# Optimization experiments

Measured on AMD Instinct MI355X. Metric: run time of the kernel, lower is better.

## Reference

```python
import jax, jax.numpy as jnp
import numpy as np

# Model config (matches init_kwargs)
DATA_L = 256
LATENT_L = 64
LATENT_N = 8
N_COMPS = 8
LOG_2PI = float(np.log(2.0 * np.pi))


def setup_inputs() -> dict:
    key = jax.random.key(0)
    ks = jax.random.split(key, 7)
    B = 2048
    N = B * LATENT_N  # 16384
    x = jax.random.normal(ks[0], (B, DATA_L), dtype=jnp.float32)
    W_e = jax.random.normal(ks[1], (DATA_L, LATENT_L * N_COMPS * 3), dtype=jnp.float32) * 0.05
    b_e = jnp.zeros((LATENT_L * N_COMPS * 3,), dtype=jnp.float32)
    W_d = jax.random.normal(ks[2], (LATENT_L, DATA_L * N_COMPS * 3), dtype=jnp.float32) * 0.05
    b_d = jnp.zeros((DATA_L * N_COMPS * 3,), dtype=jnp.float32)
    u_e = jax.random.normal(ks[3], (N, LATENT_L), dtype=jnp.float32)
    r = jax.random.uniform(ks[4], (N, LATENT_L), dtype=jnp.float32)
    return {"x": x, "W_e": W_e, "b_e": b_e, "W_d": W_d, "b_d": b_d, "u_e": u_e, "r": r}


def _split3(pred, K, D):
    # pred: (N, 3*K*D) -> m, logp, loga each (N, K, D)
    m = pred[:, : K * D].reshape(-1, K, D)
    logp = pred[:, K * D : 2 * K * D].reshape(-1, K, D)
    loga = pred[:, 2 * K * D :].reshape(-1, K, D)
    loga = jax.nn.log_softmax(loga, axis=1)  # loga - logsumexp over comps
    return m, logp, loga


def _discrete_sample(loga, r):
    # loga: (N, K, D), r: (N, D). Matches torch: idx = sum((r > cumsum(p)).int(), dim=1)
    c = jnp.cumsum(jnp.exp(loga), axis=1)  # (N, K, D)
    idx = jnp.sum((r[:, None, :] > c).astype(jnp.int32), axis=1)  # (N, D)
    return jnp.clip(idx, 0, loga.shape[1] - 1)


def reference(x, W_e, b_e, W_d, b_d, u_e, r):
    K, L, D = N_COMPS, LATENT_L, DATA_L
    x_rep = jnp.tile(x, (LATENT_N, 1))  # (N, D)

    # Encoder (KAN with width=[data_l, 3*K*L] modeled as dense layer)
    pred_e = x_rep @ W_e + b_e  # (N, 3*K*L)
    m_e, logp_e, loga_e = _split3(pred_e, K, L)

    # Sample mixture component per (row, latent dim), gather, reparameterize
    idx = _discrete_sample(loga_e, r)  # (N, L) int32
    m_sel = jnp.take_along_axis(m_e, idx[:, None, :], axis=1)[:, 0, :]  # (N, L)
    logp_sel = jnp.take_along_axis(logp_e, idx[:, None, :], axis=1)[:, 0, :]
    h = m_sel + jnp.exp(-0.5 * logp_sel) * u_e  # (N, L)

    # log q(h|x): mixture-of-Gaussians density at h
    uh = jnp.exp(0.5 * logp_e) * (h[:, None, :] - m_e)  # (N, K, L)
    L_e = jax.nn.logsumexp(loga_e - 0.5 * uh * uh + 0.5 * logp_e, axis=1)  # (N, L)
    L_e = -0.5 * L * LOG_2PI + jnp.sum(L_e, axis=1)  # (N,)

    # log prior N(0, I)
    L_q = -0.5 * L * LOG_2PI - 0.5 * jnp.sum(h * h, axis=1)  # (N,)

    # Decoder mixture likelihood of x
    pred_d = h @ W_d + b_d  # (N, 3*K*D)
    m_d, logp_d, loga_d = _split3(pred_d, K, D)
    ux = jnp.exp(0.5 * logp_d) * (x_rep[:, None, :] - m_d)  # (N, K, D)
    L_d = jax.nn.logsumexp(loga_d - 0.5 * ux * ux + 0.5 * logp_d, axis=1)  # (N, D)
    L_d = -0.5 * D * LOG_2PI + jnp.sum(L_d, axis=1)  # (N,)

    return -jnp.mean(L_d + L_q - L_e)
```

## Files before the change

kernel.cpp:

```cpp
#include <hip/hip_runtime.h>
#include <hip/hip_bf16.h>
#include <math.h>

#define D_L   256
#define L_L   64
#define K_C   8
#define BATCH 2048
#define NTOT  16384
#define ENC_COLS 1536
#define LOG2PI 1.8378770664093453f
#define L2E    1.4426950408889634f
#define LN2    0.6931471805599453f
#define C_HL2E 0.7213475204444817f

typedef __attribute__((ext_vector_type(8)))  short short8;
typedef __attribute__((ext_vector_type(8)))  unsigned short ushort8;
typedef __attribute__((ext_vector_type(4)))  unsigned short ushort4_;
typedef __attribute__((ext_vector_type(4)))  float float4_;
typedef __attribute__((ext_vector_type(16))) float float16_;

#if defined(__has_builtin)
#  if __has_builtin(__builtin_amdgcn_exp2f)
#    define EXP2F(x) __builtin_amdgcn_exp2f(x)
#  endif
#  if __has_builtin(__builtin_amdgcn_logf)
#    define LOG2F(x) __builtin_amdgcn_logf(x)
#  endif
#endif
#ifndef EXP2F
#  define EXP2F(x) __expf((x) * LN2)
#endif
#ifndef LOG2F
#  define LOG2F(x) (__logf(x) * L2E)
#endif

#define OFF_PE    0
#define OFF_H     (BATCH * ENC_COLS)
#define OFF_WET2  (OFF_H + NTOT * L_L / 2)
#define OFF_WDT2  (OFF_WET2 + ENC_COLS * D_L / 2)
#define OFF_ACC   (OFF_WDT2 + 6144 * 64 / 2)

#define DEC_BLOCKS (4 * (NTOT / 64))

__device__ __forceinline__ unsigned short f2bf(float f) {
  unsigned u = __float_as_uint(f);
  return (unsigned short)((u + 0x7fffu + ((u >> 16) & 1u)) >> 16);
}

__global__ __launch_bounds__(256) void k_prep(
    const float* __restrict__ We, const float* __restrict__ Wd,
    unsigned short* __restrict__ WeT2, unsigned short* __restrict__ WdT2,
    float* __restrict__ accf)
{
  const int bid = blockIdx.x, t = threadIdx.x;
  if (bid == 192) {
    if (t == 0) { accf[0] = 0.0f; *(unsigned*)(accf + 1) = 0u; }
    return;
  }

  const float* src; int C, rowbase, colbase; float scale;
  unsigned short* dst;
  if (bid < 96) {
    const int comp = bid / 12, p = (bid % 12) >> 2, dt = bid & 3;
    src = Wd; C = 6144; rowbase = 0;
    colbase = p * 2048 + comp * 256 + dt * 64;
    scale = p ? L2E : 1.0f;
    dst = WdT2 + (size_t)bid * 4096;
  } else {
    const int idx = bid - 96;
    src = We; C = ENC_COLS; rowbase = (idx & 3) * 64;
    colbase = (idx >> 2) * 64;
    scale = 1.0f;
    dst = WeT2 + (size_t)idx * 4096;
  }

  __shared__ float tile[64][65];
  {
    const int col = t & 63, w0 = t >> 6;
    #pragma unroll
    for (int i = 0; i < 16; ++i) {
      const int r = w0 + i * 4;
      tile[r][col] = src[(size_t)(rowbase + r) * C + colbase + col] * scale;
    }
  }
  __syncthreads();
  const int st = t >> 6, q = (t >> 5) & 1, c = t & 31;
  #pragma unroll
  for (int dg = 0; dg < 2; ++dg) {
    ushort8 o;
    #pragma unroll
    for (int j = 0; j < 8; ++j) o[j] = f2bf(tile[st * 16 + q * 8 + j][dg * 32 + c]);
    *(ushort8*)(dst + ((((size_t)dg * 4 + st) * 2 + q) * 32 + c) * 8) = o;
  }
}

__global__ __launch_bounds__(256) void k_enc(
    const float* __restrict__ x, const unsigned short* __restrict__ WeT2,
    const float* __restrict__ be, float* __restrict__ pe)
{
  __shared__ __align__(16) unsigned short as_[64 * 264];
  const int t = threadIdx.x;
  const int w = t >> 6, l = t & 63;
  const int col = l & 31, q = l >> 5;
  const int rg = w >> 1, dg = w & 1;
  const int m0 = blockIdx.y * 64, cblk = blockIdx.x, c0 = cblk * 64;

  {
    const int kc4 = (t & 63) * 4;
    #pragma unroll
    for (int i = 0; i < 16; ++i) {
      const int r = (t >> 6) + i * 4;
      float4_ v = *(const float4_*)(x + (size_t)(m0 + r) * D_L + kc4);
      ushort4_ o;
      o[0] = f2bf(v[0]); o[1] = f2bf(v[1]); o[2] = f2bf(v[2]); o[3] = f2bf(v[3]);
      *(ushort4_*)&as_[r * 264 + kc4] = o;
    }
  }

  const float bias = be[c0 + dg * 32 + col];
  float16_ acc;
  #pragma unroll
  for (int e = 0; e < 16; ++e) acc[e] = bias;

  __syncthreads();

  const unsigned short* arow = &as_[(rg * 32 + col) * 264 + q * 8];
  const unsigned short* bbase = WeT2 + (size_t)cblk * 16384 + dg * 2048 + l * 8;
  #pragma unroll
  for (int kc = 0; kc < 4; ++kc) {
    #pragma unroll
    for (int st = 0; st < 4; ++st) {
      short8 a = *(const short8*)(arow + kc * 64 + st * 16);
      short8 b = *(const short8*)(bbase + (size_t)kc * 4096 + st * 512);
      acc = __builtin_amdgcn_mfma_f32_32x32x16_bf16(a, b, acc, 0, 0, 0);
    }
  }
  #pragma unroll
  for (int e = 0; e < 16; ++e) {
    const int row = (e & 3) + 8 * (e >> 2) + 4 * q;
    pe[(size_t)(m0 + rg * 32 + row) * ENC_COLS + c0 + dg * 32 + col] = acc[e];
  }
}

__global__ __launch_bounds__(256) void k_enc_post(
    const float* __restrict__ pe, const float* __restrict__ ue,
    const float* __restrict__ rr, unsigned short* __restrict__ h,
    float* __restrict__ accf)
{
  const int lane = threadIdx.x & 63;
  const int w = threadIdx.x >> 6;
  const int b = blockIdx.x * 4 + w;
  const float* row = pe + (size_t)b * ENC_COLS + lane;

  float m[8], p[8], a[8];
  #pragma unroll
  for (int k = 0; k < K_C; ++k) {
    m[k] = row[k * 64]; p[k] = row[512 + k * 64]; a[k] = row[1024 + k * 64];
  }
  float amax = a[0];
  #pragma unroll
  for (int k = 1; k < K_C; ++k) amax = fmaxf(amax, a[k]);
  float sa = 0.f;
  #pragma unroll
  for (int k = 0; k < K_C; ++k) sa += __expf(a[k] - amax);
  const float lse_a = amax + __logf(sa);

  float cum[8];
  {
    float cs = 0.f;
    #pragma unroll
    for (int k = 0; k < K_C; ++k) { cs += __expf(a[k] - lse_a); cum[k] = cs; }
  }
  float ep[8];
  #pragma unroll
  for (int k = 0; k < K_C; ++k) ep[k] = __expf(p[k]);

  const int st = lane >> 4, qq = (lane >> 3) & 1, jj = lane & 7;

  float tot = 0.f;
  for (int j = 0; j < 8; ++j) {
    const int n = b + BATCH * j;
    const float rv = rr[(size_t)n * L_L + lane];
    const float uv = ue[(size_t)n * L_L + lane];
    int idx = 0;
    #pragma unroll
    for (int k = 0; k < K_C; ++k) idx += (rv > cum[k]) ? 1 : 0;
    idx = min(idx, K_C - 1);
    float msel = m[0], psel = p[0];
    #pragma unroll
    for (int k = 1; k < K_C; ++k) {
      const bool sel = (idx == k);
      msel = sel ? m[k] : msel;
      psel = sel ? p[k] : psel;
    }
    const float hv = fmaf(__expf(-0.5f * psel), uv, msel);

    const int nblk = n >> 6, rgn = (n >> 5) & 1, coln = n & 31;
    h[((((size_t)(nblk * 2 + rgn) * 4 + st) * 2 + qq) * 32 + coln) * 8 + jj] = f2bf(hv);

    float stt = 0.f;
    #pragma unroll
    for (int k = 0; k < K_C; ++k) {
      const float dd = hv - m[k];
      const float tt = a[k] + 0.5f * p[k] - 0.5f * ep[k] * dd * dd;
      stt += __expf(tt);
    }
    tot += -0.5f * hv * hv - (__logf(stt + 1e-30f) - lse_a);
  }
  #pragma unroll
  for (int off = 1; off < 64; off <<= 1) tot += __shfl_xor(tot, off, 64);
  __shared__ float red2[4];
  if (lane == 0) red2[w] = tot;
  __syncthreads();
  if (threadIdx.x == 0) atomicAdd(accf, red2[0] + red2[1] + red2[2] + red2[3]);
}

__global__ __launch_bounds__(256, 2) void k_dec(
    const unsigned short* __restrict__ hF, const float* __restrict__ x,
    const unsigned short* __restrict__ WdT2, const float* __restrict__ bd,
    float* __restrict__ accf, float* __restrict__ out)
{
  const int t = threadIdx.x;
  const int w = t >> 6, l = t & 63;
  const int col = l & 31, q = l >> 5;
  const int rg = w >> 1, dg = w & 1;
  const int dt = blockIdx.x, d0 = dt * 64;
  const int nblk = blockIdx.y, n0 = nblk * 64;
  const int colD = d0 + dg * 32 + col;

  const unsigned short* hbase = hF + ((size_t)(nblk * 2 + rg) * 4) * 512 + l * 8;
  short8 af[4];
  #pragma unroll
  for (int st = 0; st < 4; ++st) af[st] = *(const short8*)(hbase + st * 512);

  float xv[16];
  #pragma unroll
  for (int e = 0; e < 16; ++e) {
    const int rw = (e & 3) + 8 * (e >> 2) + 4 * q;
    const int n = n0 + rg * 32 + rw;
    xv[e] = x[(size_t)(n & (BATCH - 1)) * D_L + colD];
  }

  float s_a[16], s_t[16];
  #pragma unroll
  for (int e = 0; e < 16; ++e) { s_a[e] = 0.f; s_t[e] = 0.f; }

  const unsigned short* wbase = WdT2 + dg * 2048 + l * 8;

  for (int comp = 0; comp < K_C; ++comp) {
    const float bm  = bd[comp * 256 + colD];
    const float bpL = bd[2048 + comp * 256 + colD] * L2E;
    const float baL = bd[4096 + comp * 256 + colD] * L2E;

    short8 bf[3][4];
    #pragma unroll
    for (int p = 0; p < 3; ++p) {
      const unsigned short* pb = wbase + ((size_t)(comp * 3 + p) * 4 + dt) * 4096;
      #pragma unroll
      for (int st = 0; st < 4; ++st) bf[p][st] = *(const short8*)(pb + st * 512);
    }

    float16_ am = {}, ap = {}, aa = {};
    #pragma unroll
    for (int st = 0; st < 4; ++st) {
      am = __builtin_amdgcn_mfma_f32_32x32x16_bf16(af[st], bf[0][st], am, 0, 0, 0);
      ap = __builtin_amdgcn_mfma_f32_32x32x16_bf16(af[st], bf[1][st], ap, 0, 0, 0);
      aa = __builtin_amdgcn_mfma_f32_32x32x16_bf16(af[st], bf[2][st], aa, 0, 0, 0);
    }

    #pragma unroll
    for (int e = 0; e < 16; ++e) {
      const float dd  = xv[e] - (am[e] + bm);
      const float lpL = ap[e] + bpL;
      const float laL = aa[e] + baL;
      const float ex2 = EXP2F(lpL);
      const float t1  = fmaf(0.5f, lpL, laL);
      const float ttL = fmaf(-C_HL2E * ex2, dd * dd, t1);
      s_a[e] += EXP2F(laL);
      s_t[e] += EXP2F(ttL);
    }
  }

  float v = 0.f;
  #pragma unroll
  for (int e = 0; e < 16; ++e)
    v += LOG2F(s_t[e] + 1e-30f) - LOG2F(s_a[e]);
  v *= LN2;
  #pragma unroll
  for (int off = 1; off < 64; off <<= 1) v += __shfl_xor(v, off, 64);
  __shared__ float red[4];
  if (l == 0) red[w] = v;
  __syncthreads();
  if (t == 0) {
    atomicAdd(accf, red[0] + red[1] + red[2] + red[3]);
    __threadfence();
    unsigned* done = (unsigned*)(accf + 1);
    if (atomicAdd(done, 1u) == DEC_BLOCKS - 1) {
      const float tot = atomicAdd(accf, 0.0f);
      out[0] = -(tot / (float)NTOT) + 128.0f * LOG2PI;
    }
  }
}

extern "C" void kernel_launch(void* const* d_in, const int* in_sizes, int n_in,
                              void* d_out, int out_size, void* d_ws, size_t ws_size,
                              hipStream_t stream)
{
  const float* x  = (const float*)d_in[0];
  const float* We = (const float*)d_in[1];
  const float* be = (const float*)d_in[2];
  const float* Wd = (const float*)d_in[3];
  const float* bd = (const float*)d_in[4];
  const float* ue = (const float*)d_in[5];
  const float* rr = (const float*)d_in[6];
  float* out = (float*)d_out;

  float* ws = (float*)d_ws;
  float* pe            = ws + OFF_PE;
  unsigned short* h    = (unsigned short*)(ws + OFF_H);
  unsigned short* WeT2 = (unsigned short*)(ws + OFF_WET2);
  unsigned short* WdT2 = (unsigned short*)(ws + OFF_WDT2);
  float* accf          = ws + OFF_ACC;

  k_prep<<<dim3(193), 256, 0, stream>>>(We, Wd, WeT2, WdT2, accf);
  k_enc<<<dim3(ENC_COLS / 64, BATCH / 64), 256, 0, stream>>>(x, WeT2, be, pe);
  k_enc_post<<<dim3(BATCH / 4), 256, 0, stream>>>(pe, ue, rr, h, accf);
  k_dec<<<dim3(4, NTOT / 64), 256, 0, stream>>>(h, x, WdT2, bd, accf, out);
}
```

Baseline: 136.2 us.

## Prefetch next component decoder weights during epilogue and swizzle block order

```diff
diff --git a/kernel.cpp b/kernel.cpp
--- a/kernel.cpp
+++ b/kernel.cpp
@@ -224,8 +224,11 @@
   const int w = t >> 6, l = t & 63;
   const int col = l & 31, q = l >> 5;
   const int rg = w >> 1, dg = w & 1;
-  const int dt = blockIdx.x, d0 = dt * 64;
-  const int nblk = blockIdx.y, n0 = nblk * 64;
+
+  const int bid0 = blockIdx.x + 4 * blockIdx.y;
+  const int bid  = (bid0 & 7) * 128 + (bid0 >> 3);
+  const int dt = bid & 3, d0 = dt * 64;
+  const int nblk = bid >> 2, n0 = nblk * 64;
   const int colD = d0 + dg * 32 + col;
 
   const unsigned short* hbase = hF + ((size_t)(nblk * 2 + rg) * 4) * 512 + l * 8;
@@ -246,20 +249,21 @@
   for (int e = 0; e < 16; ++e) { s_a[e] = 0.f; s_t[e] = 0.f; }
 
   const unsigned short* wbase = WdT2 + dg * 2048 + l * 8;
-
+  const float* bdc = bd + colD;
+
+  short8 bf[3][4];
+  #pragma unroll
+  for (int p = 0; p < 3; ++p) {
+    const unsigned short* pb = wbase + ((size_t)p * 4 + dt) * 4096;
+    #pragma unroll
+    for (int st = 0; st < 4; ++st) bf[p][st] = *(const short8*)(pb + st * 512);
+  }
+  float bm  = bdc[0];
+  float bpL = bdc[2048] * L2E;
+  float baL = bdc[4096] * L2E;
+
+  #pragma unroll 1
   for (int comp = 0; comp < K_C; ++comp) {
-    const float bm  = bd[comp * 256 + colD];
-    const float bpL = bd[2048 + comp * 256 + colD] * L2E;
-    const float baL = bd[4096 + comp * 256 + colD] * L2E;
-
-    short8 bf[3][4];
-    #pragma unroll
-    for (int p = 0; p < 3; ++p) {
-      const unsigned short* pb = wbase + ((size_t)(comp * 3 + p) * 4 + dt) * 4096;
-      #pragma unroll
-      for (int st = 0; st < 4; ++st) bf[p][st] = *(const short8*)(pb + st * 512);
-    }
-
     float16_ am = {}, ap = {}, aa = {};
     #pragma unroll
     for (int st = 0; st < 4; ++st) {
@@ -268,11 +272,26 @@
       aa = __builtin_amdgcn_mfma_f32_32x32x16_bf16(af[st], bf[2][st], aa, 0, 0, 0);
     }
 
+    const float cbm = bm, cbpL = bpL, cbaL = baL;
+
+    if (comp + 1 < K_C) {
+      #pragma unroll
+      for (int p = 0; p < 3; ++p) {
+        const unsigned short* pb =
+            wbase + ((size_t)((comp + 1) * 3 + p) * 4 + dt) * 4096;
+        #pragma unroll
+        for (int st = 0; st < 4; ++st) bf[p][st] = *(const short8*)(pb + st * 512);
+      }
+      bm  = bdc[(comp + 1) * 256];
+      bpL = bdc[2048 + (comp + 1) * 256] * L2E;
+      baL = bdc[4096 + (comp + 1) * 256] * L2E;
+    }
+
     #pragma unroll
     for (int e = 0; e < 16; ++e) {
-      const float dd  = xv[e] - (am[e] + bm);
-      const float lpL = ap[e] + bpL;
-      const float laL = aa[e] + baL;
+      const float dd  = xv[e] - (am[e] + cbm);
+      const float lpL = ap[e] + cbpL;
+      const float laL = aa[e] + cbaL;
       const float ex2 = EXP2F(lpL);
       const float t1  = fmaf(0.5f, lpL, laL);
       const float ttL = fmaf(-C_HL2E * ex2, dd * dd, t1);
```

Measured after the change: 138.2 us. Within noise of the previous version (+1.5%).

## Replace global atomic reduction with per-block partials and a final reduce kernel

Applied to the files above, without the earlier changes.

```diff
diff --git a/kernel.cpp b/kernel.cpp
--- a/kernel.cpp
+++ b/kernel.cpp
@@ -38,9 +38,10 @@
 #define OFF_H     (BATCH * ENC_COLS)
 #define OFF_WET2  (OFF_H + NTOT * L_L / 2)
 #define OFF_WDT2  (OFF_WET2 + ENC_COLS * D_L / 2)
-#define OFF_ACC   (OFF_WDT2 + 6144 * 64 / 2)
-
-#define DEC_BLOCKS (4 * (NTOT / 64))
+
+#define PART_STRIDE 32
+#define N_PART_DEC  1024
+#define N_PART_ENC  1024
 
 __device__ __forceinline__ unsigned short f2bf(float f) {
   unsigned u = __float_as_uint(f);
@@ -49,14 +50,9 @@
 
 __global__ __launch_bounds__(256) void k_prep(
     const float* __restrict__ We, const float* __restrict__ Wd,
-    unsigned short* __restrict__ WeT2, unsigned short* __restrict__ WdT2,
-    float* __restrict__ accf)
+    unsigned short* __restrict__ WeT2, unsigned short* __restrict__ WdT2)
 {
   const int bid = blockIdx.x, t = threadIdx.x;
-  if (bid == 192) {
-    if (t == 0) { accf[0] = 0.0f; *(unsigned*)(accf + 1) = 0u; }
-    return;
-  }
 
   const float* src; int C, rowbase, colbase; float scale;
   unsigned short* dst;
@@ -145,11 +141,13 @@
 __global__ __launch_bounds__(256) void k_enc_post(
     const float* __restrict__ pe, const float* __restrict__ ue,
     const float* __restrict__ rr, unsigned short* __restrict__ h,
-    float* __restrict__ accf)
+    float* __restrict__ part)
 {
   const int lane = threadIdx.x & 63;
   const int w = threadIdx.x >> 6;
-  const int b = blockIdx.x * 4 + w;
+  const int gid = blockIdx.x * 4 + w;
+  const int b = gid >> 1;
+  const int j0 = (gid & 1) * 4;
   const float* row = pe + (size_t)b * ENC_COLS + lane;
 
   float m[8], p[8], a[8];
@@ -178,7 +176,8 @@
   const int st = lane >> 4, qq = (lane >> 3) & 1, jj = lane & 7;
 
   float tot = 0.f;
-  for (int j = 0; j < 8; ++j) {
+  for (int jr = 0; jr < 4; ++jr) {
+    const int j = j0 + jr;
     const int n = b + BATCH * j;
     const float rv = rr[(size_t)n * L_L + lane];
     const float uv = ue[(size_t)n * L_L + lane];
@@ -212,13 +211,14 @@
   __shared__ float red2[4];
   if (lane == 0) red2[w] = tot;
   __syncthreads();
-  if (threadIdx.x == 0) atomicAdd(accf, red2[0] + red2[1] + red2[2] + red2[3]);
+  if (threadIdx.x == 0)
+    part[(size_t)blockIdx.x * PART_STRIDE] = red2[0] + red2[1] + red2[2] + red2[3];
 }
 
 __global__ __launch_bounds__(256, 2) void k_dec(
     const unsigned short* __restrict__ hF, const float* __restrict__ x,
     const unsigned short* __restrict__ WdT2, const float* __restrict__ bd,
-    float* __restrict__ accf, float* __restrict__ out)
+    float* __restrict__ part)
 {
   const int t = threadIdx.x;
   const int w = t >> 6, l = t & 63;
@@ -292,14 +292,25 @@
   if (l == 0) red[w] = v;
   __syncthreads();
   if (t == 0) {
-    atomicAdd(accf, red[0] + red[1] + red[2] + red[3]);
-    __threadfence();
-    unsigned* done = (unsigned*)(accf + 1);
-    if (atomicAdd(done, 1u) == DEC_BLOCKS - 1) {
-      const float tot = atomicAdd(accf, 0.0f);
-      out[0] = -(tot / (float)NTOT) + 128.0f * LOG2PI;
-    }
-  }
+    const int bid = (blockIdx.y << 2) | blockIdx.x;
+    part[(size_t)(N_PART_ENC + bid) * PART_STRIDE] = red[0] + red[1] + red[2] + red[3];
+  }
+}
+
+__global__ __launch_bounds__(256) void k_final(
+    const float* __restrict__ part, float* __restrict__ out)
+{
+  const int t = threadIdx.x;
+  float s = 0.f;
+  #pragma unroll
+  for (int i = 0; i < 8; ++i) s += part[(size_t)(t + i * 256) * PART_STRIDE];
+  #pragma unroll
+  for (int off = 1; off < 64; off <<= 1) s += __shfl_xor(s, off, 64);
+  __shared__ float red[4];
+  if ((t & 63) == 0) red[t >> 6] = s;
+  __syncthreads();
+  if (t == 0)
+    out[0] = -((red[0] + red[1] + red[2] + red[3]) / (float)NTOT) + 128.0f * LOG2PI;
 }
 
 extern "C" void kernel_launch(void* const* d_in, const int* in_sizes, int n_in,
@@ -320,10 +331,11 @@
   unsigned short* h    = (unsigned short*)(ws + OFF_H);
   unsigned short* WeT2 = (unsigned short*)(ws + OFF_WET2);
   unsigned short* WdT2 = (unsigned short*)(ws + OFF_WDT2);
-  float* accf          = ws + OFF_ACC;
-
-  k_prep<<<dim3(193), 256, 0, stream>>>(We, Wd, WeT2, WdT2, accf);
+  float* part          = ws + OFF_WET2;
+
+  k_prep<<<dim3(192), 256, 0, stream>>>(We, Wd, WeT2, WdT2);
   k_enc<<<dim3(ENC_COLS / 64, BATCH / 64), 256, 0, stream>>>(x, WeT2, be, pe);
-  k_enc_post<<<dim3(BATCH / 4), 256, 0, stream>>>(pe, ue, rr, h, accf);
-  k_dec<<<dim3(4, NTOT / 64), 256, 0, stream>>>(h, x, WdT2, bd, accf, out);
-}
+  k_enc_post<<<dim3(BATCH / 2), 256, 0, stream>>>(pe, ue, rr, h, part);
+  k_dec<<<dim3(4, NTOT / 64), 256, 0, stream>>>(h, x, WdT2, bd, part);
+  k_final<<<dim3(1), 256, 0, stream>>>(part, out);
+}
```

Result: faster. 119.4 us (-12.4%).
